# Kernel optimization log

Measured on AMD Instinct MI355X. Metric: run time of the kernel, lower is better.

## Reference

```python
import jax, jax.numpy as jnp
import numpy as np

B, N, H = 8, 2048, 128


def setup_inputs() -> dict:
    key = jax.random.key(0)
    ks = jax.random.split(key, 8)
    s = 1.0 / np.sqrt(H)
    return {
        "h": jax.random.normal(ks[0], (B, N, H), dtype=jnp.float32),
        "A": jax.random.uniform(ks[1], (B, N, N), dtype=jnp.float32),
        "W1": jax.random.normal(ks[2], (H, H), dtype=jnp.float32) * s,
        "b1": jnp.zeros((H,), dtype=jnp.float32),
        "W2": jax.random.normal(ks[3], (H, H), dtype=jnp.float32) * s,
        "b2": jnp.zeros((H,), dtype=jnp.float32),
        "W_ih": jax.random.normal(ks[4], (3 * H, H), dtype=jnp.float32) * s,
        "W_hh": jax.random.normal(ks[5], (3 * H, H), dtype=jnp.float32) * s,
        "b_ih": jnp.zeros((3 * H,), dtype=jnp.float32),
        "b_hh": jnp.zeros((3 * H,), dtype=jnp.float32),
    }


def reference(h, A, W1, b1, W2, b2, W_ih, W_hh, b_ih, b_hh):
    # message MLP: two Linear+ReLU layers (n-layer embedding with act)
    m = jax.nn.relu(jnp.einsum('bnh,oh->bno', h, W1) + b1)
    m = jax.nn.relu(jnp.einsum('bnh,oh->bno', m, W2) + b2)
    # adjacency aggregation + activation
    msg = jax.nn.relu(jnp.einsum('bnm,bmh->bnh', A, m))
    # GRU vertex update: input = msg, state = h (torch GRUCell gate order r,z,n)
    gx = jnp.einsum('bnh,oh->bno', msg, W_ih) + b_ih   # [B,N,3H]
    gh = jnp.einsum('bnh,oh->bno', h, W_hh) + b_hh     # [B,N,3H]
    gx_r, gx_z, gx_n = jnp.split(gx, 3, axis=-1)
    gh_r, gh_z, gh_n = jnp.split(gh, 3, axis=-1)
    r = jax.nn.sigmoid(gx_r + gh_r)
    z = jax.nn.sigmoid(gx_z + gh_z)
    n = jnp.tanh(gx_n + r * gh_n)
    return (1.0 - z) * n + z * h
```

## Files before the change

### kernel.cpp

```cpp
#include <hip/hip_runtime.h>
#include <hip/hip_bf16.h>
#include <math.h>

#define BB 8
#define NN 2048
#define HH 128
#define BN (BB*NN)

typedef unsigned short ushort_t;
typedef __attribute__((ext_vector_type(8))) short short8_t;
typedef __attribute__((ext_vector_type(4))) float f32x4_t;

#define WS_FLAG   0
#define WS_W1H    4096
#define WS_W1L    (WS_W1H + 32768)
#define WS_W2H    (WS_W1L + 32768)
#define WS_W2L    (WS_W2H + 32768)
#define WS_WIHH   (WS_W2L + 32768)
#define WS_WIHL   (WS_WIHH + 98304)
#define WS_WHHH   (WS_WIHL + 98304)
#define WS_WHHL   (WS_WHHH + 98304)
#define WS_B1     (WS_WHHL + 98304)
#define WS_B2     (WS_B1 + 512)
#define WS_BIH    (WS_B2 + 512)
#define WS_BHH    (WS_BIH + 1536)
#define WS_M      532480
#define WS_MLO    (WS_M + 4194304)

template<bool BF16>
__device__ __forceinline__ float ldf(const void* p, size_t off) {
    if constexpr (BF16) return (float)((const __bf16*)p)[off];
    else                return ((const float*)p)[off];
}

__device__ __forceinline__ float f4c(const float4 v, int i) {
    switch (i) { case 0: return v.x; case 1: return v.y; case 2: return v.z; default: return v.w; }
}

__device__ __forceinline__ ushort_t bf_rn(float v) {
    __bf16 b = (__bf16)v;
    return *(ushort_t*)&b;
}
__device__ __forceinline__ float bf_to_f(ushort_t u) {
    return __uint_as_float((unsigned)u << 16);
}
__device__ __forceinline__ float bfs_to_f(short s) {
    return __uint_as_float(((unsigned)(ushort_t)s) << 16);
}
__device__ __forceinline__ void split2(float v, ushort_t& hi, ushort_t& lo) {
    hi = bf_rn(v);
    lo = bf_rn(v - bf_to_f(hi));
}

__device__ __forceinline__ f32x4_t mfma16(short8_t a, short8_t b, f32x4_t c) {
    return __builtin_amdgcn_mfma_f32_16x16x32_bf16(a, b, c, 0, 0, 0);
}

__global__ void detect_kernel(const ushort_t* __restrict__ Au, int* __restrict__ flag)
{
    __shared__ int cnt;
    if (threadIdx.x == 0) cnt = 0;
    __syncthreads();
    int c = 0;
    for (int i = threadIdx.x; i < 4096; i += 256)
        if (Au[i] > 0x3F80u) ++c;
    atomicAdd(&cnt, c);
    __syncthreads();
    if (threadIdx.x == 0) *flag = (cnt < 100) ? 1 : 0;
}

template<bool BF16>
__device__ void prep_body(
    const void* W1, const void* b1, const void* W2, const void* b2,
    const void* Wih, const void* Whh, const void* bih, const void* bhh,
    char* ws)
{
    ushort_t* w1h = (ushort_t*)(ws + WS_W1H);
    ushort_t* w1l = (ushort_t*)(ws + WS_W1L);
    ushort_t* w2h = (ushort_t*)(ws + WS_W2H);
    ushort_t* w2l = (ushort_t*)(ws + WS_W2L);
    ushort_t* wihh = (ushort_t*)(ws + WS_WIHH);
    ushort_t* wihl = (ushort_t*)(ws + WS_WIHL);
    ushort_t* whhh = (ushort_t*)(ws + WS_WHHH);
    ushort_t* whhl = (ushort_t*)(ws + WS_WHHL);
    float* b1f  = (float*)(ws + WS_B1);
    float* b2f  = (float*)(ws + WS_B2);
    float* bihf = (float*)(ws + WS_BIH);
    float* bhhf = (float*)(ws + WS_BHH);

    int t = blockIdx.x * 256 + threadIdx.x;
    int nth = gridDim.x * 256;
    for (int i = t; i < HH * HH; i += nth) {
        int c = i >> 7, k = i & 127;
        int po = (((k >> 5) * 8 + (c >> 4)) * 64 + (c & 15) + 16 * ((k >> 3) & 3)) * 8 + (k & 7);
        ushort_t hi, lo;
        split2(ldf<BF16>(W1, i), hi, lo); w1h[po] = hi; w1l[po] = lo;
        split2(ldf<BF16>(W2, i), hi, lo); w2h[po] = hi; w2l[po] = lo;
    }
    for (int i = t; i < 3 * HH * HH; i += nth) {
        int c = i >> 7, k = i & 127;
        int po = (((k >> 5) * 24 + (c >> 4)) * 64 + (c & 15) + 16 * ((k >> 3) & 3)) * 8 + (k & 7);
        ushort_t hi, lo;
        split2(ldf<BF16>(Wih, i), hi, lo); wihh[po] = hi; wihl[po] = lo;
        split2(ldf<BF16>(Whh, i), hi, lo); whhh[po] = hi; whhl[po] = lo;
    }
    if (t < HH)     { b1f[t] = ldf<BF16>(b1, t);  b2f[t] = ldf<BF16>(b2, t); }
    if (t < 3 * HH) { bihf[t] = ldf<BF16>(bih, t); bhhf[t] = ldf<BF16>(bhh, t); }
}

__global__ __launch_bounds__(256) void prep_kernel(
    const int* __restrict__ flag,
    const void* W1, const void* b1, const void* W2, const void* b2,
    const void* Wih, const void* Whh, const void* bih, const void* bhh,
    char* __restrict__ ws)
{
    if (*flag) prep_body<true >(W1, b1, W2, b2, Wih, Whh, bih, bhh, ws);
    else       prep_body<false>(W1, b1, W2, b2, Wih, Whh, bih, bhh, ws);
}

template<bool BF16, bool SPLIT>
__device__ void mlp_body(char* smem, const void* h, char* ws)
{
    float    (*hf)[132]  = (float(*)[132])smem;
    ushort_t (*m1h)[264] = (ushort_t(*)[264])(smem + 16896);
    ushort_t (*m1l)[264] = (ushort_t(*)[264])(smem + 33792);

    const ushort_t* w1h = (const ushort_t*)(ws + WS_W1H);
    const ushort_t* w1l = (const ushort_t*)(ws + WS_W1L);
    const ushort_t* w2h = (const ushort_t*)(ws + WS_W2H);
    const ushort_t* w2l = (const ushort_t*)(ws + WS_W2L);
    const float* b1f = (const float*)(ws + WS_B1);
    const float* b2f = (const float*)(ws + WS_B2);
    ushort_t* mTh = (ushort_t*)(ws + WS_M);
    ushort_t* mTl = (ushort_t*)(ws + WS_MLO);

    const int tid = threadIdx.x;
    const int row0 = blockIdx.x * 32;

    if constexpr (BF16) {
#pragma unroll
        for (int j = 0; j < 2; ++j) {
            int e = j * 256 + tid;
            int r = e >> 4, c8 = (e & 15) * 8;
            short8_t v = *reinterpret_cast<const short8_t*>((const ushort_t*)h + (size_t)(row0 + r) * HH + c8);
#pragma unroll
            for (int q = 0; q < 8; ++q) hf[r][c8 + q] = bfs_to_f(v[q]);
        }
    } else {
#pragma unroll
        for (int j = 0; j < 4; ++j) {
            int e = j * 256 + tid;
            int r = e >> 5, c4 = (e & 31) * 4;
            *(float4*)&hf[r][c4] = *reinterpret_cast<const float4*>((const float*)h + (size_t)(row0 + r) * HH + c4);
        }
    }
    __syncthreads();

    const int lane = tid & 63, wv = tid >> 6;
    const int lr = lane & 15, hq = lane >> 4;
    const int rt = wv & 1, ct0 = (wv >> 1) * 4;

    f32x4_t acc[4];
#pragma unroll
    for (int c = 0; c < 4; ++c) { acc[c][0] = 0.f; acc[c][1] = 0.f; acc[c][2] = 0.f; acc[c][3] = 0.f; }

    for (int k0 = 0; k0 < HH; k0 += 32) {
        short8_t ahh, ahl;
        {
            float4 f0 = *(const float4*)&hf[rt * 16 + lr][k0 + 8 * hq];
            float4 f1 = *(const float4*)&hf[rt * 16 + lr][k0 + 8 * hq + 4];
#pragma unroll
            for (int j = 0; j < 4; ++j) {
                ushort_t hi, lo;
                split2(f4c(f0, j), hi, lo); ahh[j] = (short)hi; ahl[j] = (short)lo;
                split2(f4c(f1, j), hi, lo); ahh[j + 4] = (short)hi; ahl[j + 4] = (short)lo;
            }
        }
        const int ks = k0 >> 5;
#pragma unroll
        for (int c = 0; c < 4; ++c) {
            size_t po = ((size_t)(ks * 8 + ct0 + c)) * 512 + (size_t)lane * 8;
            short8_t bh = *reinterpret_cast<const short8_t*>(w1h + po);
            acc[c] = mfma16(ahh, bh, acc[c]);
            if constexpr (!BF16) {
                short8_t bl = *reinterpret_cast<const short8_t*>(w1l + po);
                acc[c] = mfma16(ahl, bh, acc[c]);
                acc[c] = mfma16(ahh, bl, acc[c]);
            }
        }
    }
#pragma unroll
    for (int c = 0; c < 4; ++c) {
        int col = (ct0 + c) * 16 + lr;
        float bv = b1f[col];
#pragma unroll
        for (int q = 0; q < 4; ++q) {
            int row = rt * 16 + hq * 4 + q;
            float v = fmaxf(acc[c][q] + bv, 0.f);
            ushort_t hi, lo;
            split2(v, hi, lo);
            m1h[row][col] = hi;
            if constexpr (!BF16) m1l[row][col] = lo;
        }
    }
    __syncthreads();

    f32x4_t acc2[4];
#pragma unroll
    for (int c = 0; c < 4; ++c) { acc2[c][0] = 0.f; acc2[c][1] = 0.f; acc2[c][2] = 0.f; acc2[c][3] = 0.f; }

    for (int k0 = 0; k0 < HH; k0 += 32) {
        short8_t amh = *reinterpret_cast<const short8_t*>(&m1h[rt * 16 + lr][k0 + 8 * hq]);
        short8_t aml;
        if constexpr (!BF16) aml = *reinterpret_cast<const short8_t*>(&m1l[rt * 16 + lr][k0 + 8 * hq]);
        const int ks = k0 >> 5;
#pragma unroll
        for (int c = 0; c < 4; ++c) {
            size_t po = ((size_t)(ks * 8 + ct0 + c)) * 512 + (size_t)lane * 8;
            short8_t bh = *reinterpret_cast<const short8_t*>(w2h + po);
            acc2[c] = mfma16(amh, bh, acc2[c]);
            if constexpr (!BF16) {
                short8_t bl = *reinterpret_cast<const short8_t*>(w2l + po);
                acc2[c] = mfma16(aml, bh, acc2[c]);
                acc2[c] = mfma16(amh, bl, acc2[c]);
            }
        }
    }
    {
        const int bb = row0 >> 11, nb = row0 & 2047;
#pragma unroll
        for (int c = 0; c < 4; ++c) {
            int col = (ct0 + c) * 16 + lr;
            float bv = b2f[col];
#pragma unroll
            for (int q = 0; q < 4; ++q) {
                int nn = nb + rt * 16 + hq * 4 + q;
                float v = fmaxf(acc2[c][q] + bv, 0.f);
                ushort_t hi, lo;
                split2(v, hi, lo);
                size_t po = (((size_t)(bb * 64 + (nn >> 5)) * 8 + (ct0 + c)) * 64
                             + lr + 16 * ((nn >> 3) & 3)) * 8 + (nn & 7);
                mTh[po] = hi;
                if constexpr (SPLIT) mTl[po] = lo;
            }
        }
    }
}

template<bool SPLIT>
__global__ __launch_bounds__(256) void mlp_kernel(
    const int* __restrict__ flag, const void* __restrict__ h, char* __restrict__ ws)
{
    __shared__ __align__(16) char smem[50688];
    if (*flag) mlp_body<true, false>(smem, h, ws);
    else       mlp_body<false, SPLIT>(smem, h, ws);
}

template<bool BF16, bool SPLIT>
__device__ void msg_body(char* smem, const void* A, const char* ws, void* out)
{
    ushort_t (*As_h)[72] = (ushort_t(*)[72])smem;
    ushort_t (*As_l)[72] = (ushort_t(*)[72])(smem + 4608);
    const ushort_t* mThp = (const ushort_t*)(ws + WS_M);
    const ushort_t* mTlp = (const ushort_t*)(ws + WS_MLO);

    const int tid = threadIdx.x;
    const int b = blockIdx.x & 7, rtile = blockIdx.x >> 3;
    const int n0 = rtile * 32;
    const int lane = tid & 63, wv = tid >> 6;
    const int lr = lane & 15, hq = lane >> 4;
    const int wr = (wv & 1) * 16, wc4 = (wv >> 1) * 4;

    f32x4_t acc[4];
#pragma unroll
    for (int t = 0; t < 4; ++t) { acc[t][0] = 0.f; acc[t][1] = 0.f; acc[t][2] = 0.f; acc[t][3] = 0.f; }

    const int er0 = tid >> 4, ec0 = (tid & 15) * 4;
    const int br_ = tid >> 3, bc_ = (tid & 7) * 8;

    float4 ar0, ar1;
    short8_t abr;

    auto loadA = [&](int kt) {
        if constexpr (BF16) {
            abr = *reinterpret_cast<const short8_t*>(
                (const ushort_t*)A + ((size_t)(b * NN + n0 + br_)) * NN + kt * 64 + bc_);
        } else {
            const float* ap = (const float*)A;
            ar0 = *reinterpret_cast<const float4*>(ap + ((size_t)(b * NN + n0 + er0)) * NN + kt * 64 + ec0);
            ar1 = *reinterpret_cast<const float4*>(ap + ((size_t)(b * NN + n0 + er0 + 16)) * NN + kt * 64 + ec0);
        }
    };
    auto writeA = [&]() {
        if constexpr (BF16) {
            *reinterpret_cast<short8_t*>(&As_h[br_][bc_]) = abr;
        } else {
            ushort4 h4, l4;
            split2(ar0.x, h4.x, l4.x); split2(ar0.y, h4.y, l4.y);
            split2(ar0.z, h4.z, l4.z); split2(ar0.w, h4.w, l4.w);
            *reinterpret_cast<ushort4*>(&As_h[er0][ec0]) = h4;
            *reinterpret_cast<ushort4*>(&As_l[er0][ec0]) = l4;
            split2(ar1.x, h4.x, l4.x); split2(ar1.y, h4.y, l4.y);
            split2(ar1.z, h4.z, l4.z); split2(ar1.w, h4.w, l4.w);
            *reinterpret_cast<ushort4*>(&As_h[er0 + 16][ec0]) = h4;
            *reinterpret_cast<ushort4*>(&As_l[er0 + 16][ec0]) = l4;
        }
    };

    loadA(0);
    for (int kt = 0; kt < 32; ++kt) {
        writeA();
        __syncthreads();
        if (kt + 1 < 32) loadA(kt + 1);
#pragma unroll
        for (int kh = 0; kh < 2; ++kh) {
            short8_t ah = *reinterpret_cast<const short8_t*>(&As_h[wr + lr][kh * 32 + 8 * hq]);
            short8_t al;
            if constexpr (!BF16) al = *reinterpret_cast<const short8_t*>(&As_l[wr + lr][kh * 32 + 8 * hq]);
            const size_t pb = ((size_t)(b * 64 + kt * 2 + kh) * 8 + wc4) * 512 + (size_t)lane * 8;
            short8_t bh[4], bl[4];
#pragma unroll
            for (int t = 0; t < 4; ++t)
                bh[t] = *reinterpret_cast<const short8_t*>(mThp + pb + t * 512);
            if constexpr (!BF16 && SPLIT) {
#pragma unroll
                for (int t = 0; t < 4; ++t)
                    bl[t] = *reinterpret_cast<const short8_t*>(mTlp + pb + t * 512);
            }
#pragma unroll
            for (int t = 0; t < 4; ++t) {
                acc[t] = mfma16(ah, bh[t], acc[t]);
                if constexpr (!BF16) {
                    acc[t] = mfma16(al, bh[t], acc[t]);
                    if constexpr (SPLIT) acc[t] = mfma16(ah, bl[t], acc[t]);
                }
            }
        }
        __syncthreads();
    }

    char* ob = (char*)out;
    const int wc = wc4 * 16;
#pragma unroll
    for (int t = 0; t < 4; ++t)
#pragma unroll
        for (int q = 0; q < 4; ++q) {
            int row = wr + hq * 4 + q, col = wc + t * 16 + lr;
            size_t gr = (size_t)(b * NN + n0 + row);
            float v = fmaxf(acc[t][q], 0.f);
            if constexpr (BF16) {
                *(ushort_t*)(ob + gr * 256 + col * 2) = bf_rn(v);
            } else {
                ushort_t hi, lo;
                split2(v, hi, lo);
                *(ushort_t*)(ob + gr * 512 + col * 2) = hi;
                *(ushort_t*)(ob + gr * 512 + 256 + col * 2) = lo;
            }
        }
}

template<bool SPLIT>
__global__ __launch_bounds__(256) void msg_kernel(
    const int* __restrict__ flag, const void* __restrict__ A,
    const char* __restrict__ ws, void* __restrict__ out)
{
    __shared__ __align__(16) char smem[9216];
    if (*flag) msg_body<true, false>(smem, A, (const char*)ws, out);
    else       msg_body<false, SPLIT>(smem, A, (const char*)ws, out);
}

template<bool BF16>
__device__ void gru_body(char* smem, const void* h, const char* ws, void* out)
{
    ushort_t (*msgh)[264] = (ushort_t(*)[264])smem;
    ushort_t (*msgl)[264] = (ushort_t(*)[264])(smem + 16896);
    float    (*hf)[132]   = (float(*)[132])(smem + 33792);

    const ushort_t* wihh = (const ushort_t*)(ws + WS_WIHH);
    const ushort_t* wihl = (const ushort_t*)(ws + WS_WIHL);
    const ushort_t* whhh = (const ushort_t*)(ws + WS_WHHH);
    const ushort_t* whhl = (const ushort_t*)(ws + WS_WHHL);
    const float* bihf = (const float*)(ws + WS_BIH);
    const float* bhhf = (const float*)(ws + WS_BHH);

    const int tid = threadIdx.x;
    const int row0 = blockIdx.x * 32;
    char* ob = (char*)out;

    if constexpr (BF16) {
#pragma unroll
        for (int j = 0; j < 2; ++j) {
            int e = j * 256 + tid;
            int r = e >> 4, c8 = (e & 15) * 8;
            short8_t v = *reinterpret_cast<const short8_t*>(ob + (size_t)(row0 + r) * 256 + c8 * 2);
            *(short8_t*)&msgh[r][c8] = v;
        }
    } else {
#pragma unroll
        for (int j = 0; j < 4; ++j) {
            int e = j * 256 + tid;
            int r = e >> 5, off = (e & 31) * 16;
            short8_t v = *reinterpret_cast<const short8_t*>(ob + (size_t)(row0 + r) * 512 + off);
            if (off < 256) *(short8_t*)&msgh[r][off >> 1] = v;
            else           *(short8_t*)&msgl[r][(off - 256) >> 1] = v;
        }
    }
    if constexpr (BF16) {
#pragma unroll
        for (int j = 0; j < 2; ++j) {
            int e = j * 256 + tid;
            int r = e >> 4, c8 = (e & 15) * 8;
            short8_t v = *reinterpret_cast<const short8_t*>((const ushort_t*)h + (size_t)(row0 + r) * HH + c8);
#pragma unroll
            for (int q = 0; q < 8; ++q) hf[r][c8 + q] = bfs_to_f(v[q]);
        }
    } else {
#pragma unroll
        for (int j = 0; j < 4; ++j) {
            int e = j * 256 + tid;
            int r = e >> 5, c4 = (e & 31) * 4;
            *(float4*)&hf[r][c4] = *reinterpret_cast<const float4*>((const float*)h + (size_t)(row0 + r) * HH + c4);
        }
    }
    __syncthreads();

    const int lane = tid & 63, wv = tid >> 6;
    const int lr = lane & 15, hq = lane >> 4;
    const int cw0 = wv * 32;

    f32x4_t accx[2][3][2], acch[2][3][2];
#pragma unroll
    for (int rt = 0; rt < 2; ++rt)
#pragma unroll
        for (int g = 0; g < 3; ++g)
#pragma unroll
            for (int ct = 0; ct < 2; ++ct) {
                accx[rt][g][ct][0] = 0.f; accx[rt][g][ct][1] = 0.f;
                accx[rt][g][ct][2] = 0.f; accx[rt][g][ct][3] = 0.f;
                acch[rt][g][ct][0] = 0.f; acch[rt][g][ct][1] = 0.f;
                acch[rt][g][ct][2] = 0.f; acch[rt][g][ct][3] = 0.f;
            }

    for (int k0 = 0; k0 < HH; k0 += 32) {
        short8_t amh[2], aml[2], ahh[2], ahl[2];
#pragma unroll
        for (int rt = 0; rt < 2; ++rt) {
            amh[rt] = *reinterpret_cast<const short8_t*>(&msgh[rt * 16 + lr][k0 + 8 * hq]);
            if constexpr (!BF16)
                aml[rt] = *reinterpret_cast<const short8_t*>(&msgl[rt * 16 + lr][k0 + 8 * hq]);
            float4 f0 = *(const float4*)&hf[rt * 16 + lr][k0 + 8 * hq];
            float4 f1 = *(const float4*)&hf[rt * 16 + lr][k0 + 8 * hq + 4];
#pragma unroll
            for (int j = 0; j < 4; ++j) {
                ushort_t hi, lo;
                split2(f4c(f0, j), hi, lo); ahh[rt][j] = (short)hi; ahl[rt][j] = (short)lo;
                split2(f4c(f1, j), hi, lo); ahh[rt][j + 4] = (short)hi; ahl[rt][j + 4] = (short)lo;
            }
        }
        const int ks = k0 >> 5;
#pragma unroll
        for (int g = 0; g < 3; ++g)
#pragma unroll
            for (int ct = 0; ct < 2; ++ct) {
                const size_t po = ((size_t)(ks * 24 + g * 8 + wv * 2 + ct)) * 512 + (size_t)lane * 8;
                short8_t bxh  = *reinterpret_cast<const short8_t*>(wihh + po);
                short8_t bhh2 = *reinterpret_cast<const short8_t*>(whhh + po);
                short8_t bxl, bhl2;
                if constexpr (!BF16) {
                    bxl  = *reinterpret_cast<const short8_t*>(wihl + po);
                    bhl2 = *reinterpret_cast<const short8_t*>(whhl + po);
                }
#pragma unroll
                for (int rt = 0; rt < 2; ++rt) {
                    accx[rt][g][ct] = mfma16(amh[rt], bxh, accx[rt][g][ct]);
                    acch[rt][g][ct] = mfma16(ahh[rt], bhh2, acch[rt][g][ct]);
                    if constexpr (!BF16) {
                        accx[rt][g][ct] = mfma16(aml[rt], bxh, accx[rt][g][ct]);
                        accx[rt][g][ct] = mfma16(amh[rt], bxl, accx[rt][g][ct]);
                        acch[rt][g][ct] = mfma16(ahl[rt], bhh2, acch[rt][g][ct]);
                        acch[rt][g][ct] = mfma16(ahh[rt], bhl2, acch[rt][g][ct]);
                    }
                }
            }
    }

#pragma unroll
    for (int rt = 0; rt < 2; ++rt)
#pragma unroll
        for (int ct = 0; ct < 2; ++ct) {
            int col = cw0 + ct * 16 + lr;
            float brx = bihf[col],       brh = bhhf[col];
            float bzx = bihf[128 + col], bzh = bhhf[128 + col];
            float bnx = bihf[256 + col], bnh = bhhf[256 + col];
#pragma unroll
            for (int q = 0; q < 4; ++q) {
                int row = rt * 16 + hq * 4 + q;
                float gr_ = (accx[rt][0][ct][q] + brx) + (acch[rt][0][ct][q] + brh);
                float gz_ = (accx[rt][1][ct][q] + bzx) + (acch[rt][1][ct][q] + bzh);
                float gxn = accx[rt][2][ct][q] + bnx;
                float ghn = acch[rt][2][ct][q] + bnh;
                float rr = 1.f / (1.f + expf(-gr_));
                float zz = 1.f / (1.f + expf(-gz_));
                float nv = tanhf(gxn + rr * ghn);
                float hv = hf[row][col];
                float res = (1.f - zz) * nv + zz * hv;
                size_t o = (size_t)(row0 + row) * HH + col;
                if constexpr (BF16) ((ushort_t*)out)[o] = bf_rn(res);
                else                ((float*)out)[o]    = res;
            }
        }
}

__global__ __launch_bounds__(256) __attribute__((amdgpu_waves_per_eu(1, 2)))
void gru_kernel(
    const int* __restrict__ flag, const void* __restrict__ h,
    const char* __restrict__ ws, void* __restrict__ out)
{
    __shared__ __align__(16) char smem[50688];
    if (*flag) gru_body<true >(smem, h, (const char*)ws, out);
    else       gru_body<false>(smem, h, (const char*)ws, out);
}

__global__ void diag_kernel(float* __restrict__ out, float val, int nfill)
{
    int i = blockIdx.x * 256 + threadIdx.x;
    if (i < nfill) out[i] = val;
}

extern "C" void kernel_launch(void* const* d_in, const int* in_sizes, int n_in,
                              void* d_out, int out_size, void* d_ws, size_t ws_size,
                              hipStream_t stream)
{
    const int expected[10] = {BN * HH, BB * NN * NN, HH * HH, HH, HH * HH, HH,
                              3 * HH * HH, 3 * HH * HH, 3 * HH, 3 * HH};
    int bad = -1;
    if (n_in < 10) bad = 50;
    else {
        for (int i = 0; i < 10; ++i)
            if (in_sizes[i] != expected[i]) { bad = i; break; }
    }
    if (bad < 0 && out_size != BN * HH) bad = 60;
    if (bad >= 0) {
        float val = 10000.0f + 1000.0f * (float)bad;
        int nfill = out_size / 2;
        diag_kernel<<<(nfill + 255) / 256, 256, 0, stream>>>((float*)d_out, val, nfill);
        return;
    }

    const void* h   = d_in[0];
    const void* A   = d_in[1];
    const void* W1  = d_in[2];
    const void* b1  = d_in[3];
    const void* W2  = d_in[4];
    const void* b2  = d_in[5];
    const void* Wih = d_in[6];
    const void* Whh = d_in[7];
    const void* bih = d_in[8];
    const void* bhh = d_in[9];

    const size_t need_bf  = WS_M + (size_t)BN * HH * 2;
    const size_t need_f32 = WS_M + (size_t)BN * HH * 4;
    if (ws_size < need_bf) {
        float val = 2000.0f + (float)(ws_size >> 10);
        int nfill = out_size / 2;
        diag_kernel<<<(nfill + 255) / 256, 256, 0, stream>>>((float*)d_out, val, nfill);
        return;
    }
    const bool split = (ws_size >= need_f32);
    int*  flag = (int*)d_ws;
    char* ws   = (char*)d_ws;

    detect_kernel<<<1, 256, 0, stream>>>((const ushort_t*)A, flag);
    prep_kernel<<<64, 256, 0, stream>>>(flag, W1, b1, W2, b2, Wih, Whh, bih, bhh, ws);

    if (split) {
        mlp_kernel<true ><<<BN / 32, 256, 0, stream>>>(flag, h, ws);
        msg_kernel<true ><<<BB * (NN / 32), 256, 0, stream>>>(flag, A, ws, d_out);
    } else {
        mlp_kernel<false><<<BN / 32, 256, 0, stream>>>(flag, h, ws);
        msg_kernel<false><<<BB * (NN / 32), 256, 0, stream>>>(flag, A, ws, d_out);
    }
    gru_kernel<<<BN / 32, 256, 0, stream>>>(flag, h, ws, d_out);
}
```

Measured before the change: 316.9 us.

## Pipeline A loads with double-buffered LDS, fuse detect into prep, stage output stores

Merges the dtype-detect kernel into the weight-prep kernel, so each block recomputes the flag itself and one launch is removed. The message aggregation kernel now keeps four A tiles in flight in registers and double-buffers them in LDS, which drops one barrier per k-step and hides global load latency behind the MFMAs. The output is staged through LDS so each row is written with coalesced 16-byte stores instead of scattered 2-byte ones. In exchange it uses more registers and twice the LDS, which can reduce occupancy.

```diff
diff --git a/kernel.cpp b/kernel.cpp
--- a/kernel.cpp
+++ b/kernel.cpp
@@ -56,17 +56,10 @@
     return __builtin_amdgcn_mfma_f32_16x16x32_bf16(a, b, c, 0, 0, 0);
 }
 
-__global__ void detect_kernel(const ushort_t* __restrict__ Au, int* __restrict__ flag)
-{
-    __shared__ int cnt;
-    if (threadIdx.x == 0) cnt = 0;
-    __syncthreads();
-    int c = 0;
-    for (int i = threadIdx.x; i < 4096; i += 256)
-        if (Au[i] > 0x3F80u) ++c;
-    atomicAdd(&cnt, c);
-    __syncthreads();
-    if (threadIdx.x == 0) *flag = (cnt < 100) ? 1 : 0;
+__device__ __forceinline__ void lds_barrier() {
+    asm volatile("s_waitcnt lgkmcnt(0)" ::: "memory");
+    __builtin_amdgcn_s_barrier();
+    __builtin_amdgcn_sched_barrier(0);
 }
 
 template<bool BF16>
@@ -109,13 +102,23 @@
 }
 
 __global__ __launch_bounds__(256) void prep_kernel(
-    const int* __restrict__ flag,
+    const ushort_t* __restrict__ Au,
     const void* W1, const void* b1, const void* W2, const void* b2,
     const void* Wih, const void* Whh, const void* bih, const void* bhh,
-    char* __restrict__ ws)
-{
-    if (*flag) prep_body<true >(W1, b1, W2, b2, Wih, Whh, bih, bhh, ws);
-    else       prep_body<false>(W1, b1, W2, b2, Wih, Whh, bih, bhh, ws);
+    char* __restrict__ ws, int* __restrict__ flag)
+{
+    __shared__ int cnt;
+    if (threadIdx.x == 0) cnt = 0;
+    __syncthreads();
+    int c = 0;
+    for (int i = threadIdx.x; i < 4096; i += 256)
+        if (Au[i] > 0x3F80u) ++c;
+    atomicAdd(&cnt, c);
+    __syncthreads();
+    const bool isbf = (cnt < 100);
+    if (blockIdx.x == 0 && threadIdx.x == 0) *flag = isbf ? 1 : 0;
+    if (isbf) prep_body<true >(W1, b1, W2, b2, Wih, Whh, bih, bhh, ws);
+    else      prep_body<false>(W1, b1, W2, b2, Wih, Whh, bih, bhh, ws);
 }
 
 template<bool BF16, bool SPLIT>
@@ -259,8 +262,8 @@
 template<bool BF16, bool SPLIT>
 __device__ void msg_body(char* smem, const void* A, const char* ws, void* out)
 {
-    ushort_t (*As_h)[72] = (ushort_t(*)[72])smem;
-    ushort_t (*As_l)[72] = (ushort_t(*)[72])(smem + 4608);
+    ushort_t (*Ah)[32][72] = (ushort_t(*)[32][72])smem;
+    ushort_t (*Al)[32][72] = (ushort_t(*)[32][72])(smem + 9216);
     const ushort_t* mThp = (const ushort_t*)(ws + WS_M);
     const ushort_t* mTlp = (const ushort_t*)(ws + WS_MLO);
 
@@ -278,45 +281,52 @@
     const int er0 = tid >> 4, ec0 = (tid & 15) * 4;
     const int br_ = tid >> 3, bc_ = (tid & 7) * 8;
 
-    float4 ar0, ar1;
-    short8_t abr;
-
-    auto loadA = [&](int kt) {
+    short8_t rB[4];
+    float4   rF0[4], rF1[4];
+
+    auto issue = [&](int t) {
+        int slot = t & 3;
         if constexpr (BF16) {
-            abr = *reinterpret_cast<const short8_t*>(
-                (const ushort_t*)A + ((size_t)(b * NN + n0 + br_)) * NN + kt * 64 + bc_);
+            rB[slot] = *reinterpret_cast<const short8_t*>(
+                (const ushort_t*)A + ((size_t)(b * NN + n0 + br_)) * NN + t * 64 + bc_);
         } else {
             const float* ap = (const float*)A;
-            ar0 = *reinterpret_cast<const float4*>(ap + ((size_t)(b * NN + n0 + er0)) * NN + kt * 64 + ec0);
-            ar1 = *reinterpret_cast<const float4*>(ap + ((size_t)(b * NN + n0 + er0 + 16)) * NN + kt * 64 + ec0);
+            rF0[slot] = *reinterpret_cast<const float4*>(ap + ((size_t)(b * NN + n0 + er0)) * NN + t * 64 + ec0);
+            rF1[slot] = *reinterpret_cast<const float4*>(ap + ((size_t)(b * NN + n0 + er0 + 16)) * NN + t * 64 + ec0);
         }
     };
-    auto writeA = [&]() {
+    auto stage = [&](int t) {
+        int slot = t & 3, buf = t & 1;
         if constexpr (BF16) {
-            *reinterpret_cast<short8_t*>(&As_h[br_][bc_]) = abr;
+            *reinterpret_cast<short8_t*>(&Ah[buf][br_][bc_]) = rB[slot];
         } else {
             ushort4 h4, l4;
-            split2(ar0.x, h4.x, l4.x); split2(ar0.y, h4.y, l4.y);
-            split2(ar0.z, h4.z, l4.z); split2(ar0.w, h4.w, l4.w);
-            *reinterpret_cast<ushort4*>(&As_h[er0][ec0]) = h4;
-            *reinterpret_cast<ushort4*>(&As_l[er0][ec0]) = l4;
-            split2(ar1.x, h4.x, l4.x); split2(ar1.y, h4.y, l4.y);
-            split2(ar1.z, h4.z, l4.z); split2(ar1.w, h4.w, l4.w);
-            *reinterpret_cast<ushort4*>(&As_h[er0 + 16][ec0]) = h4;
-            *reinterpret_cast<ushort4*>(&As_l[er0 + 16][ec0]) = l4;
+            float4 v = rF0[slot];
+            split2(v.x, h4.x, l4.x); split2(v.y, h4.y, l4.y);
+            split2(v.z, h4.z, l4.z); split2(v.w, h4.w, l4.w);
+            *reinterpret_cast<ushort4*>(&Ah[buf][er0][ec0]) = h4;
+            *reinterpret_cast<ushort4*>(&Al[buf][er0][ec0]) = l4;
+            v = rF1[slot];
+            split2(v.x, h4.x, l4.x); split2(v.y, h4.y, l4.y);
+            split2(v.z, h4.z, l4.z); split2(v.w, h4.w, l4.w);
+            *reinterpret_cast<ushort4*>(&Ah[buf][er0 + 16][ec0]) = h4;
+            *reinterpret_cast<ushort4*>(&Al[buf][er0 + 16][ec0]) = l4;
         }
     };
 
-    loadA(0);
+    issue(0); issue(1);
+    stage(0);
+    issue(2); issue(3);
+    lds_barrier();
+
     for (int kt = 0; kt < 32; ++kt) {
-        writeA();
-        __syncthreads();
-        if (kt + 1 < 32) loadA(kt + 1);
+        if (kt + 1 < 32) stage(kt + 1);
+        const int cur = kt & 1;
 #pragma unroll
         for (int kh = 0; kh < 2; ++kh) {
-            short8_t ah = *reinterpret_cast<const short8_t*>(&As_h[wr + lr][kh * 32 + 8 * hq]);
+            short8_t ah = *reinterpret_cast<const short8_t*>(&Ah[cur][wr + lr][kh * 32 + 8 * hq]);
             short8_t al;
-            if constexpr (!BF16) al = *reinterpret_cast<const short8_t*>(&As_l[wr + lr][kh * 32 + 8 * hq]);
+            if constexpr (!BF16) al = *reinterpret_cast<const short8_t*>(&Al[cur][wr + lr][kh * 32 + 8 * hq]);
             const size_t pb = ((size_t)(b * 64 + kt * 2 + kh) * 8 + wc4) * 512 + (size_t)lane * 8;
             short8_t bh[4], bl[4];
 #pragma unroll
@@ -327,6 +337,7 @@
                 for (int t = 0; t < 4; ++t)
                     bl[t] = *reinterpret_cast<const short8_t*>(mTlp + pb + t * 512);
             }
+            if (kh == 0 && kt + 4 < 32) issue(kt + 4);
 #pragma unroll
             for (int t = 0; t < 4; ++t) {
                 acc[t] = mfma16(ah, bh[t], acc[t]);
@@ -336,27 +347,49 @@
                 }
             }
         }
-        __syncthreads();
-    }
-
-    char* ob = (char*)out;
+        lds_barrier();
+    }
+
+    ushort_t (*Sh)[136] = (ushort_t(*)[136])smem;
+    ushort_t (*Sl)[136] = (ushort_t(*)[136])(smem + 8704);
     const int wc = wc4 * 16;
 #pragma unroll
     for (int t = 0; t < 4; ++t)
 #pragma unroll
         for (int q = 0; q < 4; ++q) {
             int row = wr + hq * 4 + q, col = wc + t * 16 + lr;
-            size_t gr = (size_t)(b * NN + n0 + row);
             float v = fmaxf(acc[t][q], 0.f);
             if constexpr (BF16) {
-                *(ushort_t*)(ob + gr * 256 + col * 2) = bf_rn(v);
+                Sh[row][col] = bf_rn(v);
             } else {
                 ushort_t hi, lo;
                 split2(v, hi, lo);
-                *(ushort_t*)(ob + gr * 512 + col * 2) = hi;
-                *(ushort_t*)(ob + gr * 512 + 256 + col * 2) = lo;
-            }
-        }
+                Sh[row][col] = hi;
+                Sl[row][col] = lo;
+            }
+        }
+    __syncthreads();
+
+    char* ob = (char*)out;
+    if constexpr (BF16) {
+#pragma unroll
+        for (int j = 0; j < 2; ++j) {
+            int c = j * 256 + tid;
+            int row = c >> 4, o16 = c & 15;
+            short8_t v = *reinterpret_cast<const short8_t*>(&Sh[row][o16 * 8]);
+            *reinterpret_cast<short8_t*>(ob + (size_t)(b * NN + n0 + row) * 256 + o16 * 16) = v;
+        }
+    } else {
+#pragma unroll
+        for (int j = 0; j < 4; ++j) {
+            int c = j * 256 + tid;
+            int row = c >> 5, rem = c & 31;
+            int half = rem >> 4, o16 = rem & 15;
+            const ushort_t* src = half ? &Sl[row][o16 * 8] : &Sh[row][o16 * 8];
+            short8_t v = *reinterpret_cast<const short8_t*>(src);
+            *reinterpret_cast<short8_t*>(ob + (size_t)(b * NN + n0 + row) * 512 + half * 256 + o16 * 16) = v;
+        }
+    }
 }
 
 template<bool SPLIT>
@@ -364,7 +397,7 @@
     const int* __restrict__ flag, const void* __restrict__ A,
     const char* __restrict__ ws, void* __restrict__ out)
 {
-    __shared__ __align__(16) char smem[9216];
+    __shared__ __align__(16) char smem[18432];
     if (*flag) msg_body<true, false>(smem, A, (const char*)ws, out);
     else       msg_body<false, SPLIT>(smem, A, (const char*)ws, out);
 }
@@ -570,8 +603,8 @@
     int*  flag = (int*)d_ws;
     char* ws   = (char*)d_ws;
 
-    detect_kernel<<<1, 256, 0, stream>>>((const ushort_t*)A, flag);
-    prep_kernel<<<64, 256, 0, stream>>>(flag, W1, b1, W2, b2, Wih, Whh, bih, bhh, ws);
+    prep_kernel<<<64, 256, 0, stream>>>((const ushort_t*)A, W1, b1, W2, b2,
+                                        Wih, Whh, bih, bhh, ws, flag);
 
     if (split) {
         mlp_kernel<true ><<<BN / 32, 256, 0, stream>>>(flag, h, ws);
```

Result: slower. 337.6 us (+6.5%).
